# Kernel tuning notes

Measured on AMD Instinct MI355X. Metric: run time of the kernel, lower is better.

The kernel has to match this reference:

```python
import jax, jax.numpy as jnp
import numpy as np

EMBED_DIM = 1024
NUM_HEADS = 16
HEAD_DIM = EMBED_DIM // NUM_HEADS
SCALE = HEAD_DIM ** -0.5
B, S = 4, 2048


def setup_inputs() -> dict:
    key = jax.random.key(0)
    ks = jax.random.split(key, 11)
    std = EMBED_DIM ** -0.5
    return {
        "query": jax.random.normal(ks[0], (B, S, EMBED_DIM), jnp.float32),
        "key": jax.random.normal(ks[1], (B, S, EMBED_DIM), jnp.float32),
        "value": jax.random.normal(ks[2], (B, S, EMBED_DIM), jnp.float32),
        "Wq": jax.random.normal(ks[3], (EMBED_DIM, EMBED_DIM), jnp.float32) * std,
        "bq": jax.random.normal(ks[4], (EMBED_DIM,), jnp.float32) * 0.01,
        "Wk": jax.random.normal(ks[5], (EMBED_DIM, EMBED_DIM), jnp.float32) * std,
        "bk": jax.random.normal(ks[6], (EMBED_DIM,), jnp.float32) * 0.01,
        "Wv": jax.random.normal(ks[7], (EMBED_DIM, EMBED_DIM), jnp.float32) * std,
        "bv": jax.random.normal(ks[8], (EMBED_DIM,), jnp.float32) * 0.01,
        "Wo": jax.random.normal(ks[9], (EMBED_DIM, EMBED_DIM), jnp.float32) * std,
        "bo": jax.random.normal(ks[10], (EMBED_DIM,), jnp.float32) * 0.01,
    }


def reference(query, key, value, Wq, bq, Wk, bk, Wv, bv, Wo, bo):
    b, s, _ = query.shape
    # torch.nn.Linear: x @ W.T + b
    q = query @ Wq.T + bq
    k = key @ Wk.T + bk
    v = value @ Wv.T + bv
    # [b, h, s, d]
    q = q.reshape(b, s, NUM_HEADS, HEAD_DIM).transpose(0, 2, 1, 3)
    k = k.reshape(b, s, NUM_HEADS, HEAD_DIM).transpose(0, 2, 1, 3)
    v = v.reshape(b, s, NUM_HEADS, HEAD_DIM).transpose(0, 2, 1, 3)
    # explicit scores [b, h, s, s]
    scores = jnp.einsum("bhqd,bhkd->bhqk", q, k) * SCALE
    causal = jnp.tril(jnp.ones((s, s), dtype=bool))  # is_causal=True
    scores = jnp.where(causal, scores, -jnp.inf)
    attn = jax.nn.softmax(scores, axis=-1)
    out = jnp.einsum("bhqk,bhkd->bhqd", attn, v)
    out = out.transpose(0, 2, 1, 3).reshape(b, s, EMBED_DIM)
    return out @ Wo.T + bo
```

## Files before the change

### kernel.cpp

```cpp
#include <hip/hip_runtime.h>


#define E 1024
#define HEADS 16
#define HD 64
#define SEQ 2048
#define BATCH 4
#define MROWS (BATCH * SEQ)

typedef __bf16 bf16x8 __attribute__((ext_vector_type(8)));
typedef __bf16 bf16x4 __attribute__((ext_vector_type(4)));
typedef __bf16 bf16x2 __attribute__((ext_vector_type(2)));
typedef float f32x4 __attribute__((ext_vector_type(4)));
typedef short short4v __attribute__((ext_vector_type(4)));
typedef unsigned short ushort8v __attribute__((ext_vector_type(8)));

typedef __attribute__((address_space(1))) void gvoid;
typedef __attribute__((address_space(3))) void lvoid;

__device__ __forceinline__ void async16(const void* g, void* l) {
  __builtin_amdgcn_global_load_lds((gvoid*)g, (lvoid*)l, 16, 0, 0);
}

__device__ __forceinline__ unsigned short f2bf(float f) {
  union { float f; unsigned int u; } v;
  v.f = f;
  unsigned int r = v.u + 0x7FFFu + ((v.u >> 16) & 1u);
  return (unsigned short)(r >> 16);
}

__device__ __forceinline__ f32x4 mfma16(bf16x4 a, bf16x4 b, f32x4 c) {
  return __builtin_amdgcn_mfma_f32_16x16x16bf16_1k(
      __builtin_bit_cast(short4v, a), __builtin_bit_cast(short4v, b), c, 0, 0, 0);
}

__device__ __forceinline__ void store_out(unsigned short* p, float v) { *p = f2bf(v); }
__device__ __forceinline__ void store_out(float* p, float v) { *p = v; }

struct CastArgs {
  const float* src[4];
  unsigned short* dst[4];
  int n;
};

__global__ __launch_bounds__(256) void cast_kernel(CastArgs a) {
  const float* s = a.src[blockIdx.z];
  unsigned short* d = a.dst[blockIdx.z];
  const int n = a.n;
  const int stride = gridDim.x * blockDim.x * 4;
  for (int i = (blockIdx.x * blockDim.x + threadIdx.x) * 4; i < n; i += stride) {
    float4 v = *(const float4*)(s + i);
    ushort4 o;
    o.x = f2bf(v.x); o.y = f2bf(v.y); o.z = f2bf(v.z); o.w = f2bf(v.w);
    *(ushort4*)(d + i) = o;
  }
}

template <typename OutT>
__device__ __forceinline__ void gemm_body(const unsigned short* __restrict__ A,
                                          const unsigned short* __restrict__ W,
                                          const float* __restrict__ bias,
                                          OutT* __restrict__ out, float scale) {
  __shared__ unsigned short At[128 * 64];
  __shared__ unsigned short Wt[128 * 64];
  const int tid = threadIdx.x;
  const int lane = tid & 63;
  const int wv = tid >> 6;
  const int wm = wv & 1, wn = wv >> 1;
  const int li = lane & 15, g = lane >> 4;
  const int m0 = blockIdx.x * 128, n0 = blockIdx.y * 128;
  f32x4 acc[4][4] = {};

  for (int k0 = 0; k0 < E; k0 += 64) {
    __syncthreads();
#pragma unroll
    for (int i = 0; i < 4; ++i) {
      int c = tid + 256 * i;
      int row = c >> 3, slot = c & 7;
      int gc = slot ^ (row & 7);
      async16(A + (size_t)(m0 + row) * E + k0 + gc * 8, &At[c * 8]);
      async16(W + (size_t)(n0 + row) * E + k0 + gc * 8, &Wt[c * 8]);
    }
    asm volatile("s_waitcnt vmcnt(0)" ::: "memory");
    __syncthreads();
#pragma unroll
    for (int kk = 0; kk < 2; ++kk) {
      bf16x8 af[4], bfr[4];
#pragma unroll
      for (int mt = 0; mt < 4; ++mt) {
        int r = wm * 64 + mt * 16 + li;
        int slot = (kk * 4 + g) ^ (r & 7);
        af[mt] = *(const bf16x8*)&At[r * 64 + slot * 8];
      }
#pragma unroll
      for (int nt = 0; nt < 4; ++nt) {
        int r = wn * 64 + nt * 16 + li;
        int slot = (kk * 4 + g) ^ (r & 7);
        bfr[nt] = *(const bf16x8*)&Wt[r * 64 + slot * 8];
      }
#pragma unroll
      for (int mt = 0; mt < 4; ++mt)
#pragma unroll
        for (int nt = 0; nt < 4; ++nt)
          acc[mt][nt] =
              __builtin_amdgcn_mfma_f32_16x16x32_bf16(af[mt], bfr[nt], acc[mt][nt], 0, 0, 0);
    }
  }

#pragma unroll
  for (int nt = 0; nt < 4; ++nt) {
    int col = n0 + wn * 64 + nt * 16 + li;
    float bv = bias[col];
#pragma unroll
    for (int mt = 0; mt < 4; ++mt) {
#pragma unroll
      for (int r = 0; r < 4; ++r) {
        int row = m0 + wm * 64 + mt * 16 + g * 4 + r;
        store_out(&out[(size_t)row * E + col], (acc[mt][nt][r] + bv) * scale);
      }
    }
  }
}

struct QkvArgs {
  const unsigned short* A[3];
  const unsigned short* W[3];
  const float* bias[3];
  unsigned short* out[3];
  float scale[3];
};

__global__ __launch_bounds__(256) void gemm_qkv(QkvArgs p) {
  const int z = blockIdx.z;
  gemm_body<unsigned short>(p.A[z], p.W[z], p.bias[z], p.out[z], p.scale[z]);
}

__global__ __launch_bounds__(256) void gemm_out_k(const unsigned short* __restrict__ A,
                                                  const unsigned short* __restrict__ W,
                                                  const float* __restrict__ bias,
                                                  float* __restrict__ out) {
  gemm_body<float>(A, W, bias, out, 1.0f);
}

__global__ __launch_bounds__(512, 2) void flash_kernel(const unsigned short* __restrict__ Qb,
                                                       const unsigned short* __restrict__ Kb,
                                                       const unsigned short* __restrict__ Vb,
                                                       unsigned short* __restrict__ Ob) {
  __shared__ unsigned short Kt[2][128 * 64];
  __shared__ unsigned short Vt[2][64 * 128];
  const int p = blockIdx.x;
  const int bh = blockIdx.y;
  const int b = bh >> 4, h16 = bh & 15;
  const size_t base = (size_t)b * SEQ * E + (size_t)h16 * HD;
  const unsigned short* Qp = Qb + base;
  const unsigned short* Kp = Kb + base;
  const unsigned short* Vp = Vb + base;
  unsigned short* Op = Ob + base;
  const int tid = threadIdx.x, lane = tid & 63, wv = tid >> 6;
  const int li = lane & 15, g = lane >> 4;
  const int qlo = p, qhi = 15 - p;

  bf16x8 qfL[2], qfH[2];
#pragma unroll
  for (int kk = 0; kk < 2; ++kk) {
    int rl = qlo * 128 + wv * 16 + li;
    int rh = qhi * 128 + wv * 16 + li;
    qfL[kk] = *(const bf16x8*)(Qp + (size_t)rl * E + kk * 32 + g * 8);
    qfH[kk] = *(const bf16x8*)(Qp + (size_t)rh * E + kk * 32 + g * 8);
  }

  f32x4 oaL[4] = {}, oaH[4] = {};
  float miL = -1e30f, lsL = 0.0f;
  float miH = -1e30f, lsH = 0.0f;

  ushort8v vv[2];

  auto loadV = [&](int j) {
#pragma unroll
    for (int i = 0; i < 2; ++i) {
      int c = tid + 512 * i;
      int key = c & 127, db = (c >> 7) * 8;
      vv[i] = *(const ushort8v*)(Vp + (size_t)(j * 128 + key) * E + db);
    }
  };
  auto stageK = [&](int j, int buf) {
#pragma unroll
    for (int i = 0; i < 2; ++i) {
      int c = tid + 512 * i;
      int row = c >> 3, slot = c & 7;
      int gc = slot ^ (row & 7);
      async16(Kp + (size_t)(j * 128 + row) * E + gc * 8, &Kt[buf][c * 8]);
    }
  };
  auto scatV = [&](int buf) {
#pragma unroll
    for (int i = 0; i < 2; ++i) {
      int c = tid + 512 * i;
      int key = c & 127, db = (c >> 7) * 8;
#pragma unroll
      for (int jj = 0; jj < 8; ++jj) {
        int n = db + jj;
        int slot = (key >> 3) ^ (n & 15);
        Vt[buf][n * 128 + slot * 8 + (key & 7)] = vv[i][jj];
      }
    }
  };

  auto softmax_pf = [&](f32x4 (&sacc)[4], float& mi, float& ls, f32x4 (&oa)[4],
                        bool diag, int h, bf16x4 (&pf)[4]) {
    if (diag && h * 64 + 63 > wv * 16) {
#pragma unroll
      for (int nt = 0; nt < 4; ++nt)
#pragma unroll
        for (int r = 0; r < 4; ++r) {
          int keyg = h * 64 + nt * 16 + g * 4 + r;
          int qg = wv * 16 + li;
          sacc[nt][r] = (keyg > qg) ? -1e30f : sacc[nt][r];
        }
    }
    float m4[4];
#pragma unroll
    for (int nt = 0; nt < 4; ++nt)
      m4[nt] = fmaxf(fmaxf(sacc[nt][0], sacc[nt][1]), fmaxf(sacc[nt][2], sacc[nt][3]));
    float mx = fmaxf(fmaxf(m4[0], m4[1]), fmaxf(m4[2], m4[3]));
    mx = fmaxf(mx, __shfl_xor(mx, 16));
    mx = fmaxf(mx, __shfl_xor(mx, 32));
    float mnew = fmaxf(mi, mx);
    if (!__all(mx <= mi)) {
      float alpha = __expf(mi - mnew);
      ls *= alpha;
#pragma unroll
      for (int dt = 0; dt < 4; ++dt) oa[dt] *= alpha;
    }
    mi = mnew;

    float rs4[4];
#pragma unroll
    for (int nt = 0; nt < 4; ++nt) {
      float p0 = __expf(sacc[nt][0] - mi);
      float p1 = __expf(sacc[nt][1] - mi);
      float p2 = __expf(sacc[nt][2] - mi);
      float p3 = __expf(sacc[nt][3] - mi);
      rs4[nt] = (p0 + p1) + (p2 + p3);
      bf16x4 t;
      t[0] = (__bf16)p0; t[1] = (__bf16)p1; t[2] = (__bf16)p2; t[3] = (__bf16)p3;
      pf[nt] = t;
    }
    float s = (rs4[0] + rs4[1]) + (rs4[2] + rs4[3]);
    s += __shfl_xor(s, 16);
    s += __shfl_xor(s, 32);
    ls += s;
  };

  auto compute2 = [&](bool doLo, bool diagH, bool diagL, int buf) {
#pragma unroll
    for (int h = 0; h < 2; ++h) {
      const bool skipTop = (h * 64 > wv * 16 + 15);
      const bool aH = !(diagH && skipTop);
      const bool aL = doLo && !(diagL && skipTop);
      if (!aH && !aL) continue;

      f32x4 sH[4] = {}, sL[4] = {};
#pragma unroll
      for (int kk = 0; kk < 2; ++kk) {
        bf16x8 kf[4];
#pragma unroll
        for (int nt = 0; nt < 4; ++nt) {
          int key = h * 64 + nt * 16 + li;
          int slot = (kk * 4 + g) ^ (key & 7);
          kf[nt] = *(const bf16x8*)&Kt[buf][key * 64 + slot * 8];
        }
        __builtin_amdgcn_s_setprio(1);
#pragma unroll
        for (int nt = 0; nt < 4; ++nt) {
          if (aH)
            sH[nt] = __builtin_amdgcn_mfma_f32_16x16x32_bf16(kf[nt], qfH[kk], sH[nt], 0, 0, 0);
          if (aL)
            sL[nt] = __builtin_amdgcn_mfma_f32_16x16x32_bf16(kf[nt], qfL[kk], sL[nt], 0, 0, 0);
        }
        __builtin_amdgcn_s_setprio(0);
      }

      bf16x4 pfH[4], pfL[4];
      if (aH) softmax_pf(sH, miH, lsH, oaH, diagH, h, pfH);
      if (aL) softmax_pf(sL, miL, lsL, oaL, diagL, h, pfL);

#pragma unroll
      for (int dt = 0; dt < 4; ++dt) {
        bf16x4 vf[4];
#pragma unroll
        for (int c4 = 0; c4 < 4; ++c4) {
          int c = h * 4 + c4;
          int slot = (c * 2 + (g >> 1)) ^ li;
          vf[c4] = *(const bf16x4*)&Vt[buf][(dt * 16 + li) * 128 + slot * 8 + (g & 1) * 4];
        }
        __builtin_amdgcn_s_setprio(1);
#pragma unroll
        for (int c4 = 0; c4 < 4; ++c4) {
          if (aH) oaH[dt] = mfma16(vf[c4], pfH[c4], oaH[dt]);
          if (aL) oaL[dt] = mfma16(vf[c4], pfL[c4], oaL[dt]);
        }
        __builtin_amdgcn_s_setprio(0);
      }
    }
  };

  loadV(0);
  stageK(0, 0);
  scatV(0);

  for (int j = 0; j <= qhi; ++j) {
    const int buf = j & 1;
    asm volatile("s_waitcnt vmcnt(0)" ::: "memory");
    __syncthreads();
    if (j < qhi) {
      loadV(j + 1);
      stageK(j + 1, buf ^ 1);
    }
    compute2(j <= qlo, j == qhi, j == qlo, buf);
    if (j < qhi) scatV(buf ^ 1);
  }

#pragma unroll
  for (int t = 0; t < 2; ++t) {
    const int qt = t ? qhi : qlo;
    f32x4(&oa)[4] = t ? oaH : oaL;
    float ls = t ? lsH : lsL;
    float inv = 1.0f / ls;
    int row = qt * 128 + wv * 16 + li;
#pragma unroll
    for (int dt = 0; dt < 4; ++dt) {
      ushort4 w;
      w.x = f2bf(oa[dt][0] * inv);
      w.y = f2bf(oa[dt][1] * inv);
      w.z = f2bf(oa[dt][2] * inv);
      w.w = f2bf(oa[dt][3] * inv);
      *(ushort4*)(Op + (size_t)row * E + dt * 16 + g * 4) = w;
    }
  }
}

extern "C" void kernel_launch(void* const* d_in, const int* in_sizes, int n_in,
                              void* d_out, int out_size, void* d_ws, size_t ws_size,
                              hipStream_t stream) {
  const float* q  = (const float*)d_in[0];
  const float* k  = (const float*)d_in[1];
  const float* v  = (const float*)d_in[2];
  const float* Wq = (const float*)d_in[3];
  const float* bq = (const float*)d_in[4];
  const float* Wk = (const float*)d_in[5];
  const float* bk = (const float*)d_in[6];
  const float* Wv = (const float*)d_in[7];
  const float* bv = (const float*)d_in[8];
  const float* Wo = (const float*)d_in[9];
  const float* bo = (const float*)d_in[10];

  unsigned short* Xq  = (unsigned short*)d_ws;
  unsigned short* Xk  = Xq + (size_t)MROWS * E;
  unsigned short* Xv  = Xk + (size_t)MROWS * E;
  unsigned short* Wqb = Xv + (size_t)MROWS * E;
  unsigned short* Wkb = Wqb + (size_t)E * E;
  unsigned short* Wvb = Wkb + (size_t)E * E;
  unsigned short* Wob = Wvb + (size_t)E * E;
  unsigned short* Qb  = Wob + (size_t)E * E;
  unsigned short* Kb  = Qb + (size_t)MROWS * E;
  unsigned short* Vb  = Kb + (size_t)MROWS * E;
  unsigned short* Og  = Xq;

  CastArgs ca;
  ca.src[0] = q; ca.src[1] = k; ca.src[2] = v; ca.src[3] = nullptr;
  ca.dst[0] = Xq; ca.dst[1] = Xk; ca.dst[2] = Xv; ca.dst[3] = nullptr;
  ca.n = MROWS * E;
  cast_kernel<<<dim3(1024, 1, 3), 256, 0, stream>>>(ca);

  CastArgs cw;
  cw.src[0] = Wq; cw.src[1] = Wk; cw.src[2] = Wv; cw.src[3] = Wo;
  cw.dst[0] = Wqb; cw.dst[1] = Wkb; cw.dst[2] = Wvb; cw.dst[3] = Wob;
  cw.n = E * E;
  cast_kernel<<<dim3(256, 1, 4), 256, 0, stream>>>(cw);

  QkvArgs p;
  p.A[0] = Xq;  p.A[1] = Xk;  p.A[2] = Xv;
  p.W[0] = Wqb; p.W[1] = Wkb; p.W[2] = Wvb;
  p.bias[0] = bq; p.bias[1] = bk; p.bias[2] = bv;
  p.out[0] = Qb; p.out[1] = Kb; p.out[2] = Vb;
  p.scale[0] = 0.125f; p.scale[1] = 1.0f; p.scale[2] = 1.0f;
  gemm_qkv<<<dim3(64, 8, 3), 256, 0, stream>>>(p);

  flash_kernel<<<dim3(8, 64), 512, 0, stream>>>(Qb, Kb, Vb, Og);

  gemm_out_k<<<dim3(64, 8), 256, 0, stream>>>(Og, Wob, bo, (float*)d_out);
}
```

Before: 398.2 us.

## Merge cast launches, specialize flash chunk paths, relax flash occupancy bounds

Merges the activation and weight fp32-to-bf16 casts into one seven-slice launch, removing a kernel launch. The flash attention inner chunk is split into a both-tiles path and a single-tile path, so the predicated MFMAs become unconditional code with lower register pressure. The flash kernel's launch bounds change from a fixed two blocks per CU to a waves-per-EU hint of 4 to 8, which changes how the compiler budgets registers. Duplicating the chunk code increases code size, and the new occupancy hint may cause spills or lower occupancy.

```diff
diff --git a/kernel.cpp b/kernel.cpp
--- a/kernel.cpp
+++ b/kernel.cpp
@@ -37,16 +37,16 @@
 __device__ __forceinline__ void store_out(unsigned short* p, float v) { *p = f2bf(v); }
 __device__ __forceinline__ void store_out(float* p, float v) { *p = v; }
 
-struct CastArgs {
-  const float* src[4];
-  unsigned short* dst[4];
-  int n;
+struct CastArgs7 {
+  const float* src[7];
+  unsigned short* dst[7];
+  int n[7];
 };
 
-__global__ __launch_bounds__(256) void cast_kernel(CastArgs a) {
+__global__ __launch_bounds__(256) void cast_kernel7(CastArgs7 a) {
   const float* s = a.src[blockIdx.z];
   unsigned short* d = a.dst[blockIdx.z];
-  const int n = a.n;
+  const int n = a.n[blockIdx.z];
   const int stride = gridDim.x * blockDim.x * 4;
   for (int i = (blockIdx.x * blockDim.x + threadIdx.x) * 4; i < n; i += stride) {
     float4 v = *(const float4*)(s + i);
@@ -142,10 +142,12 @@
   gemm_body<float>(A, W, bias, out, 1.0f);
 }
 
-__global__ __launch_bounds__(512, 2) void flash_kernel(const unsigned short* __restrict__ Qb,
-                                                       const unsigned short* __restrict__ Kb,
-                                                       const unsigned short* __restrict__ Vb,
-                                                       unsigned short* __restrict__ Ob) {
+__global__ __launch_bounds__(512)
+__attribute__((amdgpu_waves_per_eu(4, 8)))
+void flash_kernel(const unsigned short* __restrict__ Qb,
+                  const unsigned short* __restrict__ Kb,
+                  const unsigned short* __restrict__ Vb,
+                  unsigned short* __restrict__ Ob) {
   __shared__ unsigned short Kt[2][128 * 64];
   __shared__ unsigned short Vt[2][64 * 128];
   const int p = blockIdx.x;
@@ -252,56 +254,85 @@
     ls += s;
   };
 
-  auto compute2 = [&](bool doLo, bool diagH, bool diagL, int buf) {
-#pragma unroll
-    for (int h = 0; h < 2; ++h) {
-      const bool skipTop = (h * 64 > wv * 16 + 15);
-      const bool aH = !(diagH && skipTop);
-      const bool aL = doLo && !(diagL && skipTop);
-      if (!aH && !aL) continue;
-
-      f32x4 sH[4] = {}, sL[4] = {};
-#pragma unroll
-      for (int kk = 0; kk < 2; ++kk) {
-        bf16x8 kf[4];
-#pragma unroll
-        for (int nt = 0; nt < 4; ++nt) {
-          int key = h * 64 + nt * 16 + li;
-          int slot = (kk * 4 + g) ^ (key & 7);
-          kf[nt] = *(const bf16x8*)&Kt[buf][key * 64 + slot * 8];
-        }
-        __builtin_amdgcn_s_setprio(1);
-#pragma unroll
-        for (int nt = 0; nt < 4; ++nt) {
-          if (aH)
-            sH[nt] = __builtin_amdgcn_mfma_f32_16x16x32_bf16(kf[nt], qfH[kk], sH[nt], 0, 0, 0);
-          if (aL)
-            sL[nt] = __builtin_amdgcn_mfma_f32_16x16x32_bf16(kf[nt], qfL[kk], sL[nt], 0, 0, 0);
-        }
-        __builtin_amdgcn_s_setprio(0);
-      }
-
-      bf16x4 pfH[4], pfL[4];
-      if (aH) softmax_pf(sH, miH, lsH, oaH, diagH, h, pfH);
-      if (aL) softmax_pf(sL, miL, lsL, oaL, diagL, h, pfL);
-
-#pragma unroll
-      for (int dt = 0; dt < 4; ++dt) {
-        bf16x4 vf[4];
-#pragma unroll
-        for (int c4 = 0; c4 < 4; ++c4) {
-          int c = h * 4 + c4;
-          int slot = (c * 2 + (g >> 1)) ^ li;
-          vf[c4] = *(const bf16x4*)&Vt[buf][(dt * 16 + li) * 128 + slot * 8 + (g & 1) * 4];
-        }
-        __builtin_amdgcn_s_setprio(1);
-#pragma unroll
-        for (int c4 = 0; c4 < 4; ++c4) {
-          if (aH) oaH[dt] = mfma16(vf[c4], pfH[c4], oaH[dt]);
-          if (aL) oaL[dt] = mfma16(vf[c4], pfL[c4], oaL[dt]);
-        }
-        __builtin_amdgcn_s_setprio(0);
-      }
+  auto chunkBoth = [&](int h, int buf, bool diagH, bool diagL) {
+    f32x4 sH[4] = {}, sL[4] = {};
+#pragma unroll
+    for (int kk = 0; kk < 2; ++kk) {
+      bf16x8 kf[4];
+#pragma unroll
+      for (int nt = 0; nt < 4; ++nt) {
+        int key = h * 64 + nt * 16 + li;
+        int slot = (kk * 4 + g) ^ (key & 7);
+        kf[nt] = *(const bf16x8*)&Kt[buf][key * 64 + slot * 8];
+      }
+      __builtin_amdgcn_s_setprio(1);
+#pragma unroll
+      for (int nt = 0; nt < 4; ++nt) {
+        sH[nt] = __builtin_amdgcn_mfma_f32_16x16x32_bf16(kf[nt], qfH[kk], sH[nt], 0, 0, 0);
+        sL[nt] = __builtin_amdgcn_mfma_f32_16x16x32_bf16(kf[nt], qfL[kk], sL[nt], 0, 0, 0);
+      }
+      __builtin_amdgcn_s_setprio(0);
+    }
+
+    bf16x4 pfH[4], pfL[4];
+    softmax_pf(sH, miH, lsH, oaH, diagH, h, pfH);
+    softmax_pf(sL, miL, lsL, oaL, diagL, h, pfL);
+
+#pragma unroll
+    for (int dt = 0; dt < 4; ++dt) {
+      bf16x4 vf[4];
+#pragma unroll
+      for (int c4 = 0; c4 < 4; ++c4) {
+        int c = h * 4 + c4;
+        int slot = (c * 2 + (g >> 1)) ^ li;
+        vf[c4] = *(const bf16x4*)&Vt[buf][(dt * 16 + li) * 128 + slot * 8 + (g & 1) * 4];
+      }
+      __builtin_amdgcn_s_setprio(1);
+#pragma unroll
+      for (int c4 = 0; c4 < 4; ++c4) {
+        oaH[dt] = mfma16(vf[c4], pfH[c4], oaH[dt]);
+        oaL[dt] = mfma16(vf[c4], pfL[c4], oaL[dt]);
+      }
+      __builtin_amdgcn_s_setprio(0);
+    }
+  };
+
+  auto chunkOne = [&](const bf16x8 (&qf)[2], float& mi, float& ls, f32x4 (&oa)[4],
+                      int h, int buf, bool diag) {
+    f32x4 sacc[4] = {};
+#pragma unroll
+    for (int kk = 0; kk < 2; ++kk) {
+      bf16x8 kf[4];
+#pragma unroll
+      for (int nt = 0; nt < 4; ++nt) {
+        int key = h * 64 + nt * 16 + li;
+        int slot = (kk * 4 + g) ^ (key & 7);
+        kf[nt] = *(const bf16x8*)&Kt[buf][key * 64 + slot * 8];
+      }
+      __builtin_amdgcn_s_setprio(1);
+#pragma unroll
+      for (int nt = 0; nt < 4; ++nt)
+        sacc[nt] = __builtin_amdgcn_mfma_f32_16x16x32_bf16(kf[nt], qf[kk], sacc[nt], 0, 0, 0);
+      __builtin_amdgcn_s_setprio(0);
+    }
+
+    bf16x4 pf[4];
+    softmax_pf(sacc, mi, ls, oa, diag, h, pf);
+
+#pragma unroll
+    for (int dt = 0; dt < 4; ++dt) {
+      bf16x4 vf[4];
+#pragma unroll
+      for (int c4 = 0; c4 < 4; ++c4) {
+        int c = h * 4 + c4;
+        int slot = (c * 2 + (g >> 1)) ^ li;
+        vf[c4] = *(const bf16x4*)&Vt[buf][(dt * 16 + li) * 128 + slot * 8 + (g & 1) * 4];
+      }
+      __builtin_amdgcn_s_setprio(1);
+#pragma unroll
+      for (int c4 = 0; c4 < 4; ++c4)
+        oa[dt] = mfma16(vf[c4], pf[c4], oa[dt]);
+      __builtin_amdgcn_s_setprio(0);
     }
   };
 
@@ -317,7 +348,16 @@
       loadV(j + 1);
       stageK(j + 1, buf ^ 1);
     }
-    compute2(j <= qlo, j == qhi, j == qlo, buf);
+    const bool doLo = j <= qlo, diagH = j == qhi, diagL = j == qlo;
+#pragma unroll
+    for (int h = 0; h < 2; ++h) {
+      const bool skipTop = (h * 64 > wv * 16 + 15);
+      const bool aH = !(diagH && skipTop);
+      const bool aL = doLo && !(diagL && skipTop);
+      if (aH && aL) chunkBoth(h, buf, diagH, diagL);
+      else if (aH) chunkOne(qfH, miH, lsH, oaH, h, buf, diagH);
+      else if (aL) chunkOne(qfL, miL, lsL, oaL, h, buf, diagL);
+    }
     if (j < qhi) scatV(buf ^ 1);
   }
 
@@ -367,17 +407,15 @@
   unsigned short* Vb  = Kb + (size_t)MROWS * E;
   unsigned short* Og  = Xq;
 
-  CastArgs ca;
-  ca.src[0] = q; ca.src[1] = k; ca.src[2] = v; ca.src[3] = nullptr;
-  ca.dst[0] = Xq; ca.dst[1] = Xk; ca.dst[2] = Xv; ca.dst[3] = nullptr;
-  ca.n = MROWS * E;
-  cast_kernel<<<dim3(1024, 1, 3), 256, 0, stream>>>(ca);
-
-  CastArgs cw;
-  cw.src[0] = Wq; cw.src[1] = Wk; cw.src[2] = Wv; cw.src[3] = Wo;
-  cw.dst[0] = Wqb; cw.dst[1] = Wkb; cw.dst[2] = Wvb; cw.dst[3] = Wob;
-  cw.n = E * E;
-  cast_kernel<<<dim3(256, 1, 4), 256, 0, stream>>>(cw);
+  CastArgs7 ca;
+  ca.src[0] = q;  ca.dst[0] = Xq;  ca.n[0] = MROWS * E;
+  ca.src[1] = k;  ca.dst[1] = Xk;  ca.n[1] = MROWS * E;
+  ca.src[2] = v;  ca.dst[2] = Xv;  ca.n[2] = MROWS * E;
+  ca.src[3] = Wq; ca.dst[3] = Wqb; ca.n[3] = E * E;
+  ca.src[4] = Wk; ca.dst[4] = Wkb; ca.n[4] = E * E;
+  ca.src[5] = Wv; ca.dst[5] = Wvb; ca.n[5] = E * E;
+  ca.src[6] = Wo; ca.dst[6] = Wob; ca.n[6] = E * E;
+  cast_kernel7<<<dim3(1024, 1, 7), 256, 0, stream>>>(ca);
 
   QkvArgs p;
   p.A[0] = Xq;  p.A[1] = Xk;  p.A[2] = Xv;
```

New measurement: 546.5 us. 37.2% more time.
